# Kernel tuning notes

Hardware: AMD Instinct MI355X
Metric: run time of the kernel (lower is better)

The kernel has to match this reference:

```python
import jax, jax.numpy as jnp
import numpy as np

E = 4        # num_edge_types
C = 4        # num_channels (must equal E due to module's layer>0 einsum)
N = 2048     # num_nodes
W_IN = 256
W_OUT = 128


def _xavier_uniform(key, shape):
    # torch.nn.init.xavier_uniform_ on a 2D tensor [fan_out, fan_in] style
    fan_out, fan_in = shape[0], shape[1]
    bound = float(np.sqrt(6.0 / (fan_in + fan_out)))
    return jax.random.uniform(key, shape, jnp.float32, -bound, bound)


def setup_inputs() -> dict:
    key = jax.random.key(0)
    k = jax.random.split(key, 7)
    A = jax.random.uniform(k[0], (E, N, N), jnp.float32)   # non-negative dense multi-relation adjacency
    X = jax.random.normal(k[1], (N, W_IN), jnp.float32)
    gt_w1 = _xavier_uniform(k[2], (C, E))   # layer0 conv1
    gt_w2 = _xavier_uniform(k[3], (C, E))   # layer0 conv2
    gt_w3 = _xavier_uniform(k[4], (C, C))   # layer1 conv1 (C == E)
    gcn_w = _xavier_uniform(k[5], (W_IN, W_OUT))
    gcn_b = jnp.zeros((W_OUT,), jnp.float32)
    return {"A": A, "X": X, "gt_w1": gt_w1, "gt_w2": gt_w2, "gt_w3": gt_w3,
            "gcn_w": gcn_w, "gcn_b": gcn_b}


def _normalize_adj(adj):
    # adj: [N, N]. Symmetric degree normalization D^-1/2 (A+I) D^-1/2,
    # expressed as broadcasted row/col scaling (math-identical to the
    # original diag-matmul-matmul formulation).
    adj = adj + jnp.eye(adj.shape[0], dtype=adj.dtype)
    deg = adj.sum(axis=1)
    d = deg ** -0.5
    d = jnp.where(jnp.isinf(d), jnp.zeros_like(d), d)
    return d[:, None] * adj * d[None, :]


def reference(A, X, gt_w1, gt_w2, gt_w3, gcn_w, gcn_b):
    # --- GT layer 0 (first=True): two softmax-weighted mixes of A, then bmm ---
    fw1 = jax.nn.softmax(gt_w1, axis=1)
    fw2 = jax.nn.softmax(gt_w2, axis=1)
    Ha = jnp.einsum('oi,inm->onm', fw1, A)   # [C, N, N]
    Hb = jnp.einsum('oi,inm->onm', fw2, A)   # [C, N, N]
    H = jnp.matmul(Ha, Hb)                   # [C, N, N]
    # --- GT layer 1 (first=False): H @ (softmax mix of A) ---
    fw3 = jax.nn.softmax(gt_w3, axis=1)
    Hc = jnp.einsum('oi,inm->onm', fw3, A)   # [C, N, N]
    H = jnp.matmul(H, Hc)                    # [C, N, N]
    # --- per-channel degree-normalized GCN conv ---
    Hn = jax.vmap(_normalize_adj)(H)         # [C, N, N]
    support = X @ gcn_w                      # [N, W_OUT] (shared across channels)
    out = jnp.einsum('cnm,mf->cnf', Hn, support) + gcn_b  # [C, N, W_OUT]
    out = jax.nn.relu(out)
    # torch.cat(X_out, dim=1): channel blocks side by side -> [N, C*W_OUT]
    return jnp.transpose(out, (1, 0, 2)).reshape(N, C * W_OUT)
```

## Files before the change

kernel.cpp:

```cpp
#include <hip/hip_runtime.h>
#include <math.h>

#define N_NODES 2048
#define NNE ((long)N_NODES * N_NODES)

#define SUPD_SCALE 8192.0f

typedef _Float16 half4_t __attribute__((ext_vector_type(4)));
typedef _Float16 half8_t __attribute__((ext_vector_type(8)));
typedef float    floatx4 __attribute__((ext_vector_type(4)));

__device__ __forceinline__ void async_cp16(const void* g, void* l) {
  __builtin_amdgcn_global_load_lds((const __attribute__((address_space(1))) void*)g,
                                   (__attribute__((address_space(3))) void*)l,
                                   16, 0, 0);
}

__device__ __forceinline__ float colscale_from(float cn) {
  return exp2f((float)(10 - ilogbf(fmaxf(cn, 1e-37f))));
}

__global__ void softmax3_zero_k(const float* __restrict__ w1,
                                const float* __restrict__ w2,
                                const float* __restrict__ w3,
                                float* __restrict__ fw,
                                float* __restrict__ cn) {
  int t = threadIdx.x;
  float4 z4 = {0.f, 0.f, 0.f, 0.f};
  ((float4*)cn)[t] = z4;
  if (t < 12) {
    const float* src = (t < 4) ? w1 : (t < 8) ? w2 : w3;
    int r = t & 3;
    float v0 = src[r * 4 + 0], v1 = src[r * 4 + 1];
    float v2 = src[r * 4 + 2], v3 = src[r * 4 + 3];
    float m = fmaxf(fmaxf(v0, v1), fmaxf(v2, v3));
    float e0 = expf(v0 - m), e1 = expf(v1 - m), e2 = expf(v2 - m), e3 = expf(v3 - m);
    float inv = 1.0f / (e0 + e1 + e2 + e3);
    fw[t * 4 + 0] = e0 * inv; fw[t * 4 + 1] = e1 * inv;
    fw[t * 4 + 2] = e2 * inv; fw[t * 4 + 3] = e3 * inv;
  }
}

__global__ __launch_bounds__(128)
void support_k(const float* __restrict__ X, const float* __restrict__ W,
               float* __restrict__ sup) {
  __shared__ float Xs[256];
  const int t = threadIdx.x;
  const int m = blockIdx.x;
  Xs[t]       = X[(long)m * 256 + t];
  Xs[t + 128] = X[(long)m * 256 + t + 128];
  __syncthreads();
  float acc = 0.f;
  #pragma unroll 8
  for (int k = 0; k < 256; ++k) acc = fmaf(Xs[k], W[(long)k * 128 + t], acc);
  sup[(long)m * 128 + t] = acc;
}

__global__ __launch_bounds__(256)
void rc_from_A_k(const float* __restrict__ A, const float* __restrict__ fw,
                 float* __restrict__ rc) {
  const int wave = threadIdx.x >> 6, lane = threadIdx.x & 63;
  const int r = blockIdx.x * 4 + wave;
  float se[4];
  #pragma unroll
  for (int e = 0; e < 4; ++e) {
    const float4* row = (const float4*)(A + (long)e * NNE + (long)r * N_NODES);
    float s = 0.f;
    for (int j4 = lane; j4 < 512; j4 += 64) {
      float4 a = row[j4];
      s += (a.x + a.y) + (a.z + a.w);
    }
    for (int o = 32; o > 0; o >>= 1) s += __shfl_down(s, o, 64);
    se[e] = s;
  }
  if (lane == 0) {
    #pragma unroll
    for (int c = 0; c < 4; ++c)
      rc[c * N_NODES + r] = fw[32 + c * 4 + 0] * se[0] + fw[32 + c * 4 + 1] * se[1] +
                            fw[32 + c * 4 + 2] * se[2] + fw[32 + c * 4 + 3] * se[3];
  }
}

__global__ __launch_bounds__(256)
void matvecA_k(const float* __restrict__ A, const float* __restrict__ fw, int off,
               const float* __restrict__ vin, float* __restrict__ vout) {
  __shared__ float vs[4 * 2048];
  const int t = threadIdx.x;
  for (int i = t; i < 4 * 2048; i += 256) vs[i] = vin[i];
  __syncthreads();
  const int wave = t >> 6, lane = t & 63;
  const int r = blockIdx.x * 4 + wave;
  float acc[4][4] = {{0.f}};
  #pragma unroll
  for (int e = 0; e < 4; ++e) {
    const float4* row = (const float4*)(A + (long)e * NNE + (long)r * N_NODES);
    for (int j4 = lane; j4 < 512; j4 += 64) {
      float4 a = row[j4];
      #pragma unroll
      for (int c = 0; c < 4; ++c) {
        const float4 v = *(const float4*)&vs[c * 2048 + j4 * 4];
        acc[e][c] += (a.x * v.x + a.y * v.y) + (a.z * v.z + a.w * v.w);
      }
    }
  }
  #pragma unroll
  for (int e = 0; e < 4; ++e)
    #pragma unroll
    for (int c = 0; c < 4; ++c)
      for (int o = 32; o > 0; o >>= 1) acc[e][c] += __shfl_down(acc[e][c], o, 64);
  if (lane == 0) {
    #pragma unroll
    for (int c = 0; c < 4; ++c) {
      float s = fw[off + c * 4 + 0] * acc[0][c] + fw[off + c * 4 + 1] * acc[1][c] +
                fw[off + c * 4 + 2] * acc[2][c] + fw[off + c * 4 + 3] * acc[3][c];
      vout[c * N_NODES + r] = s;
    }
  }
}

__global__ __launch_bounds__(256)
void transposeV_k(const float* __restrict__ sup, const float* __restrict__ deg,
                  float* __restrict__ dvec, float* __restrict__ supd,
                  _Float16* __restrict__ TH, _Float16* __restrict__ TL,
                  float* __restrict__ cn0) {
  __shared__ _Float16 sh[32][33], sl[32][33];
  __shared__ float red[8][32];
  const int t = threadIdx.x;
  const int z = blockIdx.z;
  const int m0 = blockIdx.x * 32, f0 = blockIdx.y * 32;
  const int r0 = t >> 5, col = t & 31;
  float part = 0.f;
  #pragma unroll
  for (int m = 0; m < 4; ++m) {
    const int row = m0 + r0 + 8 * m;
    float dm = 1.0f / sqrtf(1.0f + deg[(long)z * N_NODES + row]);
    float sv = sup[(long)row * 128 + f0 + col] * dm;
    supd[((long)z * N_NODES + row) * 128 + f0 + col] = sv;
    if (blockIdx.y == 0 && col == 0) dvec[(long)z * N_NODES + row] = dm;
    float v = sv * SUPD_SCALE;
    _Float16 h = (_Float16)v;
    sh[r0 + 8 * m][col] = h;
    sl[r0 + 8 * m][col] = (_Float16)(v - (float)h);
    part += fabsf(v);
  }
  red[r0][col] = part;
  __syncthreads();
  if (t < 32) {
    float s = 0.f;
    #pragma unroll
    for (int q = 0; q < 8; ++q) s += red[q][t];
    atomicAdd(&cn0[(long)z * 128 + f0 + t], s);
  }
  const int rr = t >> 3, cq = (t & 7) * 4;
  half4_t oh, ol;
  #pragma unroll
  for (int d = 0; d < 4; ++d) { oh[d] = sh[cq + d][rr]; ol[d] = sl[cq + d][rr]; }
  long ob = (long)z * 128 * N_NODES + (long)(f0 + rr) * N_NODES + m0 + cq;
  *(half4_t*)(TH + ob) = oh;
  *(half4_t*)(TL + ob) = ol;
}

__global__ __launch_bounds__(256, 2)
void gemm_mix_k(const float* __restrict__ A, const float* __restrict__ fw, int off,
                const _Float16* __restrict__ BH, const _Float16* __restrict__ BL,
                float* __restrict__ C) {
  __shared__ __align__(16) _Float16 Hs[2][2][1024];
  __shared__ __align__(16) _Float16 Bs[2][2][4096];

  const int t = threadIdx.x;
  const int lane = t & 63;
  const int w = t >> 6;
  const int bid = blockIdx.x;
  const int tile = bid & 63;
  const int ch = (bid >> 6) & 3;
  const int kc = bid >> 8;
  const int i0 = tile * 32;
  const long koff = (long)kc * 1024;

  float wv[4];
  #pragma unroll
  for (int e = 0; e < 4; ++e) wv[e] = fw[off + ch * 4 + e];

  const int rr = t >> 3;
  const int k4 = (t & 7) * 4;
  const float* gA = A + (long)(i0 + rr) * N_NODES + koff + k4;
  const int hoff = rr * 32 + (((k4 >> 3) + (rr >> 1)) & 3) * 8 + (k4 & 7);

  const int hls = w >> 1;
  const int half = w & 1;
  const int kc_st = (((lane & 3) - ((lane >> 3) & 3)) & 3) * 8;
  const _Float16* gB = (hls ? BL : BH)
                     + ((long)ch * 128 + half * 64 + (lane >> 2)) * (long)N_NODES
                     + koff + kc_st;

  const int wm = w >> 1, wn = w & 1;
  const int fr = lane & 15;
  const int fq = lane >> 4;
  const int fkz = ((fq + (fr >> 1)) & 3) * 8;
  const int aoff = (wm * 16 + fr) * 32 + fkz;

  floatx4 acc[4];
  #pragma unroll
  for (int j = 0; j < 4; ++j) {
    floatx4 zz4 = {0.f, 0.f, 0.f, 0.f};
    acc[j] = zz4;
  }

  const int NKT = 32;

  auto stageB = [&](int ktv, int pb) {
    _Float16* lb = &Bs[pb][hls][half * 2048];
    const _Float16* g = gB + ktv * 32;
    #pragma unroll
    for (int q = 0; q < 4; ++q)
      async_cp16(g + (long)q * (16L * N_NODES), lb + q * 512 + lane * 8);
  };
  auto mixStore = [&](const float4& a0, const float4& a1,
                      const float4& a2, const float4& a3, int pb) {
    float av0[4] = {a0.x, a0.y, a0.z, a0.w};
    float av1[4] = {a1.x, a1.y, a1.z, a1.w};
    float av2[4] = {a2.x, a2.y, a2.z, a2.w};
    float av3[4] = {a3.x, a3.y, a3.z, a3.w};
    half4_t h, l;
    #pragma unroll
    for (int d = 0; d < 4; ++d) {
      float o = wv[0] * av0[d] + wv[1] * av1[d] + wv[2] * av2[d] + wv[3] * av3[d];
      _Float16 hh = (_Float16)o;
      h[d] = hh; l[d] = (_Float16)(o - (float)hh);
    }
    *(half4_t*)&Hs[pb][0][hoff] = h;
    *(half4_t*)&Hs[pb][1][hoff] = l;
  };

  {
    float4 a0 = *(const float4*)(gA);
    float4 a1 = *(const float4*)(gA + NNE);
    float4 a2 = *(const float4*)(gA + 2 * NNE);
    float4 a3 = *(const float4*)(gA + 3 * NNE);
    stageB(0, 0);
    mixStore(a0, a1, a2, a3, 0);
  }
  __syncthreads();

  for (int kt = 0; kt < NKT; ++kt) {
    const int p = kt & 1;
    float4 a0, a1, a2, a3;
    if (kt + 1 < NKT) {
      const float* g = gA + (kt + 1) * 32;
      a0 = *(const float4*)(g);
      a1 = *(const float4*)(g + NNE);
      a2 = *(const float4*)(g + 2 * NNE);
      a3 = *(const float4*)(g + 3 * NNE);
      stageB(kt + 1, p ^ 1);
    }
    half8_t ah = *(const half8_t*)&Hs[p][0][aoff];
    half8_t al = *(const half8_t*)&Hs[p][1][aoff];
    #pragma unroll
    for (int nt = 0; nt < 4; ++nt) {
      const int bo = (wn * 64 + nt * 16 + fr) * 32 + fkz;
      half8_t bh = *(const half8_t*)&Bs[p][0][bo];
      half8_t bl = *(const half8_t*)&Bs[p][1][bo];
      acc[nt] = __builtin_amdgcn_mfma_f32_16x16x32_f16(ah, bh, acc[nt], 0, 0, 0);
      acc[nt] = __builtin_amdgcn_mfma_f32_16x16x32_f16(al, bh, acc[nt], 0, 0, 0);
      acc[nt] = __builtin_amdgcn_mfma_f32_16x16x32_f16(ah, bl, acc[nt], 0, 0, 0);
    }
    if (kt + 1 < NKT) mixStore(a0, a1, a2, a3, p ^ 1);
    __syncthreads();
  }

  const int er = fq * 4;
  const int ec = lane & 15;
  float* Cb = C + ((long)(kc * 4 + ch) * N_NODES + i0 + wm * 16) * 128;
  #pragma unroll
  for (int nt = 0; nt < 4; ++nt) {
    const int f = wn * 64 + nt * 16 + ec;
    #pragma unroll
    for (int r = 0; r < 4; ++r)
      Cb[(long)(er + r) * 128 + f] = acc[nt][r];
  }
}

__global__ __launch_bounds__(256)
void combineT_k(const float* __restrict__ P, int parts,
                const float* __restrict__ cn_in, float* __restrict__ cn_out,
                _Float16* __restrict__ TH, _Float16* __restrict__ TL) {
  __shared__ _Float16 sh[32][33], sl[32][33];
  __shared__ float red[8][32];
  const int t = threadIdx.x;
  const int z = blockIdx.z;
  const int j0 = blockIdx.x * 32, f0 = blockIdx.y * 32;
  const int r0 = t >> 5, col = t & 31;
  const float s = colscale_from(cn_in[(long)z * 128 + f0 + col]);
  const long step = 4L * N_NODES * 128;
  float part = 0.f;
  #pragma unroll
  for (int m = 0; m < 4; ++m) {
    long idx = ((long)z * N_NODES + j0 + r0 + 8 * m) * 128 + f0 + col;
    float v = P[idx];
    for (int pp = 1; pp < parts; ++pp) v += P[idx + pp * step];
    v *= s;
    _Float16 h = (_Float16)v;
    sh[r0 + 8 * m][col] = h;
    sl[r0 + 8 * m][col] = (_Float16)(v - (float)h);
    part += fabsf(v);
  }
  if (cn_out) red[r0][col] = part;
  __syncthreads();
  if (cn_out && t < 32) {
    float ss = 0.f;
    #pragma unroll
    for (int q = 0; q < 8; ++q) ss += red[q][t];
    atomicAdd(&cn_out[(long)z * 128 + f0 + t], ss);
  }
  const int rr = t >> 3, cq = (t & 7) * 4;
  half4_t oh, ol;
  #pragma unroll
  for (int d = 0; d < 4; ++d) { oh[d] = sh[cq + d][rr]; ol[d] = sl[cq + d][rr]; }
  long ob = (long)z * 128 * N_NODES + (long)(f0 + rr) * N_NODES + j0 + cq;
  *(half4_t*)(TH + ob) = oh;
  *(half4_t*)(TL + ob) = ol;
}

__global__ __launch_bounds__(256)
void final_k(const float4* __restrict__ T2, const float4* __restrict__ supd,
             const float* __restrict__ dvec, const float* __restrict__ cn0,
             const float* __restrict__ cn1, const float* __restrict__ bias,
             float* __restrict__ out) {
  const int t = threadIdx.x;
  const int z = blockIdx.y;
  const int idx = blockIdx.x * 256 + t;
  const int i = idx >> 5;
  const int fq = (idx & 31) * 4;
  const long step4 = 4L * N_NODES * 32;
  long b4 = (long)z * N_NODES * 32 + idx;
  float4 s0 = T2[b4];
  float4 s1 = T2[b4 + step4];
  float4 sp = supd[(long)z * N_NODES * 32 + idx];
  const float dn = dvec[(long)z * N_NODES + i];
  float inv[4];
  #pragma unroll
  for (int d = 0; d < 4; ++d) {
    int i0 = ilogbf(fmaxf(cn0[(long)z * 128 + fq + d], 1e-37f));
    int i1 = ilogbf(fmaxf(cn1[(long)z * 128 + fq + d], 1e-37f));
    inv[d] = exp2f((float)(i0 + i1 - 33));
  }
  float4 o;
  o.x = fmaxf(dn * ((s0.x + s1.x) * inv[0] + sp.x) + bias[fq + 0], 0.f);
  o.y = fmaxf(dn * ((s0.y + s1.y) * inv[1] + sp.y) + bias[fq + 1], 0.f);
  o.z = fmaxf(dn * ((s0.z + s1.z) * inv[2] + sp.z) + bias[fq + 2], 0.f);
  o.w = fmaxf(dn * ((s0.w + s1.w) * inv[3] + sp.w) + bias[fq + 3], 0.f);
  *(float4*)(out + (long)i * 512 + z * 128 + fq) = o;
}

extern "C" void kernel_launch(void* const* d_in, const int* in_sizes, int n_in,
                              void* d_out, int out_size, void* d_ws, size_t ws_size,
                              hipStream_t stream) {
  const float* A  = (const float*)d_in[0];
  const float* X  = (const float*)d_in[1];
  const float* w1 = (const float*)d_in[2];
  const float* w2 = (const float*)d_in[3];
  const float* w3 = (const float*)d_in[4];
  const float* gw = (const float*)d_in[5];
  const float* gb = (const float*)d_in[6];
  float* out = (float*)d_out;

  float* ws   = (float*)d_ws;
  float* fw   = ws;
  float* rc   = fw + 64;
  float* v1   = rc + 4 * N_NODES;
  float* deg  = v1 + 4 * N_NODES;
  float* dvec = deg + 4 * N_NODES;
  float* sup  = dvec + 4 * N_NODES;
  float* cn0  = sup + (long)N_NODES * 128;
  float* cn1  = cn0 + 512;
  float* supd = cn1 + 512;
  float* Mtmp = supd + 4L * N_NODES * 128;
  _Float16* arena = (_Float16*)(Mtmp + 8L * N_NODES * 128);
  _Float16* VTH = arena;
  _Float16* VTL = VTH + 4L * 128 * N_NODES;
  _Float16* T0H = VTL + 4L * 128 * N_NODES;
  _Float16* T0L = T0H + 4L * 128 * N_NODES;
  _Float16* T1H = T0L + 4L * 128 * N_NODES;
  _Float16* T1L = T1H + 4L * 128 * N_NODES;

  softmax3_zero_k<<<1, 256, 0, stream>>>(w1, w2, w3, fw, cn0);
  support_k<<<N_NODES, 128, 0, stream>>>(X, gw, sup);
  rc_from_A_k<<<N_NODES / 4, 256, 0, stream>>>(A, fw, rc);
  matvecA_k<<<N_NODES / 4, 256, 0, stream>>>(A, fw, 16, rc, v1);
  matvecA_k<<<N_NODES / 4, 256, 0, stream>>>(A, fw, 0, v1, deg);
  transposeV_k<<<dim3(64, 4, 4), 256, 0, stream>>>(sup, deg, dvec, supd,
                                                   VTH, VTL, cn0);
  gemm_mix_k<<<512, 256, 0, stream>>>(A, fw, 32, VTH, VTL, Mtmp);
  combineT_k<<<dim3(64, 4, 4), 256, 0, stream>>>(Mtmp, 2, cn0, cn1, T0H, T0L);
  gemm_mix_k<<<512, 256, 0, stream>>>(A, fw, 16, T0H, T0L, Mtmp);
  combineT_k<<<dim3(64, 4, 4), 256, 0, stream>>>(Mtmp, 2, cn1, nullptr, T1H, T1L);
  gemm_mix_k<<<512, 256, 0, stream>>>(A, fw, 0, T1H, T1L, Mtmp);
  final_k<<<dim3(256, 4), 256, 0, stream>>>((const float4*)Mtmp,
                                            (const float4*)supd, dvec,
                                            cn0, cn1, gb, out);
}
```

Baseline: 290.4 us.

## Split GEMM K into four chunks and parallelize matvec rows across waves

The mixed-A GEMM now splits the K dimension into four 512-wide chunks instead of two, doubling the grid to 1024 blocks and raising the launch-bounds occupancy hint, with combine and final kernels summing four partials. The row-sum and matvec kernels now assign one row per block with all four waves sharing it, loading the vector directly from global memory instead of staging it in LDS, and reducing the mixed result across waves through shared memory. The aim is more parallelism and better bandwidth use on the A-streaming passes, at the cost of more partial-sum traffic and a larger workspace.

```diff
diff --git a/kernel.cpp b/kernel.cpp
--- a/kernel.cpp
+++ b/kernel.cpp
@@ -59,62 +59,83 @@
 __global__ __launch_bounds__(256)
 void rc_from_A_k(const float* __restrict__ A, const float* __restrict__ fw,
                  float* __restrict__ rc) {
-  const int wave = threadIdx.x >> 6, lane = threadIdx.x & 63;
-  const int r = blockIdx.x * 4 + wave;
+  __shared__ float red[4][4];
+  const int r = blockIdx.x;
+  const int w = threadIdx.x >> 6, lane = threadIdx.x & 63;
   float se[4];
   #pragma unroll
   for (int e = 0; e < 4; ++e) {
     const float4* row = (const float4*)(A + (long)e * NNE + (long)r * N_NODES);
     float s = 0.f;
-    for (int j4 = lane; j4 < 512; j4 += 64) {
-      float4 a = row[j4];
+    #pragma unroll
+    for (int q = 0; q < 2; ++q) {
+      float4 a = row[w * 128 + q * 64 + lane];
       s += (a.x + a.y) + (a.z + a.w);
     }
-    for (int o = 32; o > 0; o >>= 1) s += __shfl_down(s, o, 64);
     se[e] = s;
   }
+  float m[4];
+  #pragma unroll
+  for (int c = 0; c < 4; ++c)
+    m[c] = fw[32 + c * 4 + 0] * se[0] + fw[32 + c * 4 + 1] * se[1] +
+           fw[32 + c * 4 + 2] * se[2] + fw[32 + c * 4 + 3] * se[3];
+  #pragma unroll
+  for (int o = 32; o > 0; o >>= 1) {
+    #pragma unroll
+    for (int c = 0; c < 4; ++c) m[c] += __shfl_down(m[c], o, 64);
+  }
   if (lane == 0) {
     #pragma unroll
-    for (int c = 0; c < 4; ++c)
-      rc[c * N_NODES + r] = fw[32 + c * 4 + 0] * se[0] + fw[32 + c * 4 + 1] * se[1] +
-                            fw[32 + c * 4 + 2] * se[2] + fw[32 + c * 4 + 3] * se[3];
+    for (int c = 0; c < 4; ++c) red[w][c] = m[c];
+  }
+  __syncthreads();
+  if (threadIdx.x < 4) {
+    int c = threadIdx.x;
+    rc[c * N_NODES + r] = (red[0][c] + red[1][c]) + (red[2][c] + red[3][c]);
   }
 }
 
 __global__ __launch_bounds__(256)
 void matvecA_k(const float* __restrict__ A, const float* __restrict__ fw, int off,
                const float* __restrict__ vin, float* __restrict__ vout) {
-  __shared__ float vs[4 * 2048];
-  const int t = threadIdx.x;
-  for (int i = t; i < 4 * 2048; i += 256) vs[i] = vin[i];
-  __syncthreads();
-  const int wave = t >> 6, lane = t & 63;
-  const int r = blockIdx.x * 4 + wave;
+  __shared__ float red[4][4];
+  const int r = blockIdx.x;
+  const int w = threadIdx.x >> 6, lane = threadIdx.x & 63;
   float acc[4][4] = {{0.f}};
   #pragma unroll
-  for (int e = 0; e < 4; ++e) {
-    const float4* row = (const float4*)(A + (long)e * NNE + (long)r * N_NODES);
-    for (int j4 = lane; j4 < 512; j4 += 64) {
-      float4 a = row[j4];
-      #pragma unroll
-      for (int c = 0; c < 4; ++c) {
-        const float4 v = *(const float4*)&vs[c * 2048 + j4 * 4];
-        acc[e][c] += (a.x * v.x + a.y * v.y) + (a.z * v.z + a.w * v.w);
-      }
+  for (int q = 0; q < 2; ++q) {
+    const int j4 = w * 128 + q * 64 + lane;
+    float4 v0 = *(const float4*)&vin[0 * 2048 + j4 * 4];
+    float4 v1 = *(const float4*)&vin[1 * 2048 + j4 * 4];
+    float4 v2 = *(const float4*)&vin[2 * 2048 + j4 * 4];
+    float4 v3 = *(const float4*)&vin[3 * 2048 + j4 * 4];
+    #pragma unroll
+    for (int e = 0; e < 4; ++e) {
+      float4 a = *(const float4*)(A + (long)e * NNE + (long)r * N_NODES + j4 * 4);
+      acc[e][0] += (a.x * v0.x + a.y * v0.y) + (a.z * v0.z + a.w * v0.w);
+      acc[e][1] += (a.x * v1.x + a.y * v1.y) + (a.z * v1.z + a.w * v1.w);
+      acc[e][2] += (a.x * v2.x + a.y * v2.y) + (a.z * v2.z + a.w * v2.w);
+      acc[e][3] += (a.x * v3.x + a.y * v3.y) + (a.z * v3.z + a.w * v3.w);
     }
   }
-  #pragma unroll
-  for (int e = 0; e < 4; ++e)
-    #pragma unroll
-    for (int c = 0; c < 4; ++c)
-      for (int o = 32; o > 0; o >>= 1) acc[e][c] += __shfl_down(acc[e][c], o, 64);
+  float m[4];
+  #pragma unroll
+  for (int c = 0; c < 4; ++c)
+    m[c] = fw[off + c * 4 + 0] * acc[0][c] + fw[off + c * 4 + 1] * acc[1][c] +
+           fw[off + c * 4 + 2] * acc[2][c] + fw[off + c * 4 + 3] * acc[3][c];
+  #pragma unroll
+  for (int o = 32; o > 0; o >>= 1) {
+    #pragma unroll
+    for (int c = 0; c < 4; ++c) m[c] += __shfl_down(m[c], o, 64);
+  }
   if (lane == 0) {
     #pragma unroll
-    for (int c = 0; c < 4; ++c) {
-      float s = fw[off + c * 4 + 0] * acc[0][c] + fw[off + c * 4 + 1] * acc[1][c] +
-                fw[off + c * 4 + 2] * acc[2][c] + fw[off + c * 4 + 3] * acc[3][c];
-      vout[c * N_NODES + r] = s;
-    }
+    for (int c = 0; c < 4; ++c) red[w][c] = m[c];
+  }
+  __syncthreads();
+  if (threadIdx.x < 4) {
+    int c = threadIdx.x;
+    vout[c * N_NODES + r] = (red[0][c] + red[1][c]) + (red[2][c] + red[3][c]);
   }
 }
 
@@ -160,7 +181,7 @@
   *(half4_t*)(TL + ob) = ol;
 }
 
-__global__ __launch_bounds__(256, 2)
+__global__ __launch_bounds__(256, 4)
 void gemm_mix_k(const float* __restrict__ A, const float* __restrict__ fw, int off,
                 const _Float16* __restrict__ BH, const _Float16* __restrict__ BL,
                 float* __restrict__ C) {
@@ -175,7 +196,7 @@
   const int ch = (bid >> 6) & 3;
   const int kc = bid >> 8;
   const int i0 = tile * 32;
-  const long koff = (long)kc * 1024;
+  const long koff = (long)kc * 512;
 
   float wv[4];
   #pragma unroll
@@ -206,7 +227,7 @@
     acc[j] = zz4;
   }
 
-  const int NKT = 32;
+  const int NKT = 16;
 
   auto stageB = [&](int ktv, int pb) {
     _Float16* lb = &Bs[pb][hls][half * 2048];
@@ -296,8 +317,7 @@
   #pragma unroll
   for (int m = 0; m < 4; ++m) {
     long idx = ((long)z * N_NODES + j0 + r0 + 8 * m) * 128 + f0 + col;
-    float v = P[idx];
-    for (int pp = 1; pp < parts; ++pp) v += P[idx + pp * step];
+    float v = (P[idx] + P[idx + step]) + (P[idx + 2 * step] + P[idx + 3 * step]);
     v *= s;
     _Float16 h = (_Float16)v;
     sh[r0 + 8 * m][col] = h;
@@ -335,6 +355,8 @@
   long b4 = (long)z * N_NODES * 32 + idx;
   float4 s0 = T2[b4];
   float4 s1 = T2[b4 + step4];
+  float4 s2 = T2[b4 + 2 * step4];
+  float4 s3 = T2[b4 + 3 * step4];
   float4 sp = supd[(long)z * N_NODES * 32 + idx];
   const float dn = dvec[(long)z * N_NODES + i];
   float inv[4];
@@ -345,10 +367,10 @@
     inv[d] = exp2f((float)(i0 + i1 - 33));
   }
   float4 o;
-  o.x = fmaxf(dn * ((s0.x + s1.x) * inv[0] + sp.x) + bias[fq + 0], 0.f);
-  o.y = fmaxf(dn * ((s0.y + s1.y) * inv[1] + sp.y) + bias[fq + 1], 0.f);
-  o.z = fmaxf(dn * ((s0.z + s1.z) * inv[2] + sp.z) + bias[fq + 2], 0.f);
-  o.w = fmaxf(dn * ((s0.w + s1.w) * inv[3] + sp.w) + bias[fq + 3], 0.f);
+  o.x = fmaxf(dn * (((s0.x + s1.x) + (s2.x + s3.x)) * inv[0] + sp.x) + bias[fq + 0], 0.f);
+  o.y = fmaxf(dn * (((s0.y + s1.y) + (s2.y + s3.y)) * inv[1] + sp.y) + bias[fq + 1], 0.f);
+  o.z = fmaxf(dn * (((s0.z + s1.z) + (s2.z + s3.z)) * inv[2] + sp.z) + bias[fq + 2], 0.f);
+  o.w = fmaxf(dn * (((s0.w + s1.w) + (s2.w + s3.w)) * inv[3] + sp.w) + bias[fq + 3], 0.f);
   *(float4*)(out + (long)i * 512 + z * 128 + fq) = o;
 }
 
@@ -375,7 +397,7 @@
   float* cn1  = cn0 + 512;
   float* supd = cn1 + 512;
   float* Mtmp = supd + 4L * N_NODES * 128;
-  _Float16* arena = (_Float16*)(Mtmp + 8L * N_NODES * 128);
+  _Float16* arena = (_Float16*)(Mtmp + 16L * N_NODES * 128);
   _Float16* VTH = arena;
   _Float16* VTL = VTH + 4L * 128 * N_NODES;
   _Float16* T0H = VTL + 4L * 128 * N_NODES;
@@ -385,16 +407,16 @@
 
   softmax3_zero_k<<<1, 256, 0, stream>>>(w1, w2, w3, fw, cn0);
   support_k<<<N_NODES, 128, 0, stream>>>(X, gw, sup);
-  rc_from_A_k<<<N_NODES / 4, 256, 0, stream>>>(A, fw, rc);
-  matvecA_k<<<N_NODES / 4, 256, 0, stream>>>(A, fw, 16, rc, v1);
-  matvecA_k<<<N_NODES / 4, 256, 0, stream>>>(A, fw, 0, v1, deg);
+  rc_from_A_k<<<N_NODES, 256, 0, stream>>>(A, fw, rc);
+  matvecA_k<<<N_NODES, 256, 0, stream>>>(A, fw, 16, rc, v1);
+  matvecA_k<<<N_NODES, 256, 0, stream>>>(A, fw, 0, v1, deg);
   transposeV_k<<<dim3(64, 4, 4), 256, 0, stream>>>(sup, deg, dvec, supd,
                                                    VTH, VTL, cn0);
-  gemm_mix_k<<<512, 256, 0, stream>>>(A, fw, 32, VTH, VTL, Mtmp);
-  combineT_k<<<dim3(64, 4, 4), 256, 0, stream>>>(Mtmp, 2, cn0, cn1, T0H, T0L);
-  gemm_mix_k<<<512, 256, 0, stream>>>(A, fw, 16, T0H, T0L, Mtmp);
-  combineT_k<<<dim3(64, 4, 4), 256, 0, stream>>>(Mtmp, 2, cn1, nullptr, T1H, T1L);
-  gemm_mix_k<<<512, 256, 0, stream>>>(A, fw, 0, T1H, T1L, Mtmp);
+  gemm_mix_k<<<1024, 256, 0, stream>>>(A, fw, 32, VTH, VTL, Mtmp);
+  combineT_k<<<dim3(64, 4, 4), 256, 0, stream>>>(Mtmp, 4, cn0, cn1, T0H, T0L);
+  gemm_mix_k<<<1024, 256, 0, stream>>>(A, fw, 16, T0H, T0L, Mtmp);
+  combineT_k<<<dim3(64, 4, 4), 256, 0, stream>>>(Mtmp, 4, cn1, nullptr, T1H, T1L);
+  gemm_mix_k<<<1024, 256, 0, stream>>>(A, fw, 0, T1H, T1L, Mtmp);
   final_k<<<dim3(256, 4), 256, 0, stream>>>((const float4*)Mtmp,
                                             (const float4*)supd, dvec,
                                             cn0, cn1, gb, out);
```

After: 259.7 us. 10.6% less time.
